# Kernel tuning notes

Measured on AMD Instinct MI355X. Metric: run time of the kernel, lower is better.

## Reference

```python
import jax, jax.numpy as jnp
import numpy as np
import math

B, C, H = 1, 3, 224
EPS = 0.05
P_INIT = 0.8
N_QUERIES = 5000


def _p_selection(it):
    # static python schedule (rescale_schedule=False)
    if 10 < it <= 50:
        return P_INIT / 2
    elif 50 < it <= 200:
        return P_INIT / 4
    elif 200 < it <= 500:
        return P_INIT / 8
    elif 500 < it <= 1000:
        return P_INIT / 16
    elif 1000 < it <= 2000:
        return P_INIT / 32
    elif 2000 < it <= 4000:
        return P_INIT / 64
    elif 4000 < it <= 6000:
        return P_INIT / 128
    elif 6000 < it <= 8000:
        return P_INIT / 256
    elif 8000 < it:
        return P_INIT / 512
    return P_INIT


def _s_schedule():
    # patch side length per iteration; pure python -> static array
    n_features = C * H * H
    return np.array(
        [max(int(round(math.sqrt(_p_selection(i) * n_features / C))), 1) for i in range(N_QUERIES)],
        dtype=np.int32,
    )


def setup_inputs() -> dict:
    key = jax.random.key(0)
    x = jax.random.uniform(key, (B, C, H, H), dtype=jnp.float32)  # image in [0,1]
    return {"x": x}


def _forward(x):
    base = jax.random.key(1)
    # init: vertical-stripe random-sign perturbation, shape [B, C, 1, H]
    k0 = jax.random.fold_in(base, 0)
    init_sign = jnp.sign(2.0 * jax.random.uniform(k0, (x.shape[0], C, 1, H), dtype=x.dtype) - 1.0)
    x_best = jnp.clip(x + EPS * init_sign, 0.0, 1.0)

    x_lo = x - EPS
    x_hi = x + EPS
    s_arr = jnp.asarray(_s_schedule())  # [N_QUERIES] int32
    idx = jnp.arange(H)

    def step(xb, si):
        s, i = si
        k = jax.random.fold_in(base, i + 1)
        k1, k2 = jax.random.split(k)
        # vh = floor(uniform * (H - s)) in {0, ..., H-s-1}
        u = jax.random.uniform(k1, (), dtype=x.dtype)
        vh = jnp.floor(u * (H - s).astype(x.dtype)).astype(jnp.int32)
        # per-channel random sign, constant over the s x s patch
        sgn = jnp.sign(2.0 * jax.random.uniform(k2, (C, 1, 1), dtype=x.dtype) - 1.0)
        # square patch mask [H, H] at offset vh with side s (mask instead of
        # dynamic-size slice assignment; jit-friendly)
        m = (idx >= vh) & (idx < vh + s)
        mask = (m[:, None] & m[None, :]).astype(x.dtype)
        xb = xb + 2.0 * EPS * sgn * mask            # broadcasts to [B, C, H, H]
        xb = jnp.clip(jnp.minimum(jnp.maximum(xb, x_lo), x_hi), 0.0, 1.0)
        return xb, None

    x_best, _ = jax.lax.scan(step, x_best, (s_arr, jnp.arange(N_QUERIES)))
    return x_best


def reference(x):
    return _forward(x)
```

## Files before the change

### kernel.cpp

```cpp
#include <hip/hip_runtime.h>
#include <stdint.h>


#define HH 224
#define NQ 5000
#define NPIX (HH * HH)
#define EPSF 0.05f
#define NTAB (8 * 3 * 8 * 224)

__device__ __forceinline__ void tf2x32(uint32_t k0, uint32_t k1,
                                       uint32_t x0, uint32_t x1,
                                       uint32_t& o0, uint32_t& o1) {
  uint32_t ks2 = k0 ^ k1 ^ 0x1BD11BDAu;
  x0 += k0; x1 += k1;
#define TFR(r) { x0 += x1; x1 = (x1 << (r)) | (x1 >> (32 - (r))); x1 ^= x0; }
  TFR(13) TFR(15) TFR(26) TFR(6)
  x0 += k1;  x1 += ks2 + 1u;
  TFR(17) TFR(29) TFR(16) TFR(24)
  x0 += ks2; x1 += k0 + 2u;
  TFR(13) TFR(15) TFR(26) TFR(6)
  x0 += k0;  x1 += k1 + 3u;
  TFR(17) TFR(29) TFR(16) TFR(24)
  x0 += k1;  x1 += ks2 + 4u;
  TFR(13) TFR(15) TFR(26) TFR(6)
  x0 += ks2; x1 += k0 + 5u;
#undef TFR
  o0 = x0; o1 = x1;
}

__device__ __forceinline__ int sign_from_bits(uint32_t bits) {
  uint32_t mant = bits >> 9;
  return (mant > 0x400000u) ? 1 : ((mant < 0x400000u) ? -1 : 0);
}

__device__ __forceinline__ float u01_from_bits(uint32_t bits) {
  return __uint_as_float(0x3f800000u | (bits >> 9)) - 1.0f;
}

__constant__ int SEG_LO_C[8] = {0, 11, 51, 201, 501, 1001, 2001, 4001};
__constant__ int SEG_HI_C[8] = {10, 50, 200, 500, 1000, 2000, 4000, 4999};
__constant__ int SEG_SZ_C[8] = {200, 142, 100, 71, 50, 35, 25, 18};

__global__ __launch_bounds__(512) void build_kernel(uint16_t* __restrict__ gtab,
                                                    int8_t* __restrict__ gisign) {
  int blk = blockIdx.x;
  int tid = threadIdx.x;

  if (blk == 24) {
    uint32_t g0, g1;
    tf2x32(0u, 1u, 0u, 0u, g0, g1);
    for (int i = tid; i < 3 * HH; i += 512) {
      uint32_t o0, o1;
      tf2x32(g0, g1, 0u, (uint32_t)i, o0, o1);
      gisign[i] = (int8_t)sign_from_bits(o0 ^ o1);
    }
    return;
  }

  int seg = blk / 3, c = blk % 3;
  int s = SEG_SZ_C[seg];
  __shared__ uint32_t bins[224];
  __shared__ uint16_t tab[8 * 224];
  if (tid < 224) bins[tid] = 0;
  __syncthreads();

  for (int t = SEG_LO_C[seg] + tid; t <= SEG_HI_C[seg]; t += 512) {
    uint32_t f0, f1;
    tf2x32(0u, 1u, 0u, (uint32_t)(t + 1), f0, f1);
    uint32_t a0, a1, b0, b1;
    tf2x32(f0, f1, 0u, 0u, a0, a1);
    tf2x32(f0, f1, 0u, 1u, b0, b1);
    uint32_t u0, u1;
    tf2x32(a0, a1, 0u, 0u, u0, u1);
    int vh = (int)floorf(u01_from_bits(u0 ^ u1) * (float)(HH - s));
    uint32_t c0, c1;
    tf2x32(b0, b1, 0u, (uint32_t)c, c0, c1);
    int g = sign_from_bits(c0 ^ c1);
    if (g) atomicMax(&bins[vh], (((uint32_t)(t + 1)) << 1) | (uint32_t)(g > 0));
  }
  __syncthreads();

  if (tid < 224) tab[tid] = (uint16_t)bins[tid];
  __syncthreads();
  for (int k = 1; k < 8; ++k) {
    int w = 1 << (k - 1);
    if (tid < 224) {
      uint16_t a = tab[(k - 1) * 224 + tid];
      uint16_t b = (tid + w < 224) ? tab[(k - 1) * 224 + tid + w] : (uint16_t)0;
      tab[k * 224 + tid] = (a > b) ? a : b;
    }
    __syncthreads();
  }

  const uint32_t* t32 = (const uint32_t*)tab;
  uint32_t* g32 = (uint32_t*)(gtab + (seg * 3 + c) * 1792);
  for (int i = tid; i < 896; i += 512) g32[i] = t32[i];
}

__global__ __launch_bounds__(256) void resolve_kernel(const uint16_t* __restrict__ gtab,
                                                      const int8_t* __restrict__ isign,
                                                      const float* __restrict__ x,
                                                      float* __restrict__ out) {
  __shared__ uint16_t tab[NTAB];
  {
    float4* t4 = (float4*)tab;
    const float4* g4 = (const float4*)gtab;
    for (int i = threadIdx.x; i < NTAB * 2 / 16; i += 256) t4[i] = g4[i];
  }
  __syncthreads();

  int p = blockIdx.x * 256 + threadIdx.x;
  int pi = p / HH, pj = p % HH;
  int m = min(pi, pj), M = max(pi, pj);

  const int SEG_S[8] = {200, 142, 100, 71, 50, 35, 25, 18};
  uint32_t best0 = 0, best1 = 0, best2 = 0;
#pragma unroll
  for (int seg = 0; seg < 8; ++seg) {
    const int s = SEG_S[seg];
    int lo = max(0, M - s + 1);
    int hi = min(m, 223 - s);
    bool ok = (lo <= hi);
    int len = ok ? (hi - lo + 1) : 1;
    int k = 31 - __clz(len);
    int o2 = hi + 1 - (1 << k);
    int b = seg * 5376 + k * 224;
    uint32_t v0 = max((uint32_t)tab[b + lo],        (uint32_t)tab[b + o2]);
    uint32_t v1 = max((uint32_t)tab[b + 1792 + lo], (uint32_t)tab[b + 1792 + o2]);
    uint32_t v2 = max((uint32_t)tab[b + 3584 + lo], (uint32_t)tab[b + 3584 + o2]);
    if (!ok) { v0 = 0u; v1 = 0u; v2 = 0u; }
    best0 = max(best0, v0);
    best1 = max(best1, v1);
    best2 = max(best2, v2);
  }

  int s0 = best0 ? ((best0 & 1u) ? 1 : -1) : (int)isign[pj];
  int s1 = best1 ? ((best1 & 1u) ? 1 : -1) : (int)isign[HH + pj];
  int s2 = best2 ? ((best2 & 1u) ? 1 : -1) : (int)isign[2 * HH + pj];

  float x0 = x[p];
  float x1 = x[NPIX + p];
  float x2 = x[2 * NPIX + p];
  out[p]            = (s0 > 0) ? fminf(x0 + EPSF, 1.0f)
                    : (s0 < 0) ? fmaxf(x0 - EPSF, 0.0f)
                               : fminf(fmaxf(x0, 0.0f), 1.0f);
  out[NPIX + p]     = (s1 > 0) ? fminf(x1 + EPSF, 1.0f)
                    : (s1 < 0) ? fmaxf(x1 - EPSF, 0.0f)
                               : fminf(fmaxf(x1, 0.0f), 1.0f);
  out[2 * NPIX + p] = (s2 > 0) ? fminf(x2 + EPSF, 1.0f)
                    : (s2 < 0) ? fmaxf(x2 - EPSF, 0.0f)
                               : fminf(fmaxf(x2, 0.0f), 1.0f);
}

extern "C" void kernel_launch(void* const* d_in, const int* in_sizes, int n_in,
                              void* d_out, int out_size, void* d_ws, size_t ws_size,
                              hipStream_t stream) {
  const float* x = (const float*)d_in[0];
  float* out = (float*)d_out;
  uint16_t* gtab = (uint16_t*)d_ws;
  int8_t* gisign = (int8_t*)d_ws + 86016;

  build_kernel<<<25, 512, 0, stream>>>(gtab, gisign);
  resolve_kernel<<<NPIX / 256, 256, 0, stream>>>(gtab, gisign, x, out);
}
```

Baseline: 71.19 us.

## Split resolve kernel per channel and read sparse tables from global memory

The resolve kernel no longer copies the whole 86KB sparse-table set into shared memory in every block. It reads the needed entries straight from global memory, where they are expected to sit in L2. The grid gains a channel dimension, so each thread handles one channel of one pixel instead of all three. This removes the large per-block LDS fill and its barrier and raises block count and occupancy, at the cost of scattered global/L2 reads for the table lookups.

```diff
diff --git a/kernel.cpp b/kernel.cpp
--- a/kernel.cpp
+++ b/kernel.cpp
@@ -6,7 +6,6 @@
 #define NQ 5000
 #define NPIX (HH * HH)
 #define EPSF 0.05f
-#define NTAB (8 * 3 * 8 * 224)
 
 __device__ __forceinline__ void tf2x32(uint32_t k0, uint32_t k1,
                                        uint32_t x0, uint32_t x1,
@@ -101,20 +100,15 @@
                                                       const int8_t* __restrict__ isign,
                                                       const float* __restrict__ x,
                                                       float* __restrict__ out) {
-  __shared__ uint16_t tab[NTAB];
-  {
-    float4* t4 = (float4*)tab;
-    const float4* g4 = (const float4*)gtab;
-    for (int i = threadIdx.x; i < NTAB * 2 / 16; i += 256) t4[i] = g4[i];
-  }
-  __syncthreads();
-
+  int c = blockIdx.y;
   int p = blockIdx.x * 256 + threadIdx.x;
   int pi = p / HH, pj = p % HH;
   int m = min(pi, pj), M = max(pi, pj);
 
+  const uint16_t* tc = gtab + c * 1792;
+
   const int SEG_S[8] = {200, 142, 100, 71, 50, 35, 25, 18};
-  uint32_t best0 = 0, best1 = 0, best2 = 0;
+  uint32_t best = 0;
 #pragma unroll
   for (int seg = 0; seg < 8; ++seg) {
     const int s = SEG_S[seg];
@@ -125,31 +119,17 @@
     int k = 31 - __clz(len);
     int o2 = hi + 1 - (1 << k);
     int b = seg * 5376 + k * 224;
-    uint32_t v0 = max((uint32_t)tab[b + lo],        (uint32_t)tab[b + o2]);
-    uint32_t v1 = max((uint32_t)tab[b + 1792 + lo], (uint32_t)tab[b + 1792 + o2]);
-    uint32_t v2 = max((uint32_t)tab[b + 3584 + lo], (uint32_t)tab[b + 3584 + o2]);
-    if (!ok) { v0 = 0u; v1 = 0u; v2 = 0u; }
-    best0 = max(best0, v0);
-    best1 = max(best1, v1);
-    best2 = max(best2, v2);
+    uint32_t v = max((uint32_t)tc[b + lo], (uint32_t)tc[b + o2]);
+    best = max(best, ok ? v : 0u);
   }
 
-  int s0 = best0 ? ((best0 & 1u) ? 1 : -1) : (int)isign[pj];
-  int s1 = best1 ? ((best1 & 1u) ? 1 : -1) : (int)isign[HH + pj];
-  int s2 = best2 ? ((best2 & 1u) ? 1 : -1) : (int)isign[2 * HH + pj];
+  int sg = best ? ((best & 1u) ? 1 : -1) : (int)isign[c * HH + pj];
 
-  float x0 = x[p];
-  float x1 = x[NPIX + p];
-  float x2 = x[2 * NPIX + p];
-  out[p]            = (s0 > 0) ? fminf(x0 + EPSF, 1.0f)
-                    : (s0 < 0) ? fmaxf(x0 - EPSF, 0.0f)
-                               : fminf(fmaxf(x0, 0.0f), 1.0f);
-  out[NPIX + p]     = (s1 > 0) ? fminf(x1 + EPSF, 1.0f)
-                    : (s1 < 0) ? fmaxf(x1 - EPSF, 0.0f)
-                               : fminf(fmaxf(x1, 0.0f), 1.0f);
-  out[2 * NPIX + p] = (s2 > 0) ? fminf(x2 + EPSF, 1.0f)
-                    : (s2 < 0) ? fmaxf(x2 - EPSF, 0.0f)
-                               : fminf(fmaxf(x2, 0.0f), 1.0f);
+  int idx = c * NPIX + p;
+  float xv = x[idx];
+  out[idx] = (sg > 0) ? fminf(xv + EPSF, 1.0f)
+           : (sg < 0) ? fmaxf(xv - EPSF, 0.0f)
+                      : fminf(fmaxf(xv, 0.0f), 1.0f);
 }
 
 extern "C" void kernel_launch(void* const* d_in, const int* in_sizes, int n_in,
@@ -161,5 +141,6 @@
   int8_t* gisign = (int8_t*)d_ws + 86016;
 
   build_kernel<<<25, 512, 0, stream>>>(gtab, gisign);
-  resolve_kernel<<<NPIX / 256, 256, 0, stream>>>(gtab, gisign, x, out);
+  dim3 rgrid(NPIX / 256, 3);
+  resolve_kernel<<<rgrid, 256, 0, stream>>>(gtab, gisign, x, out);
 }
```

Result: faster. 66.09 us (-7.2%).
